# Performance work log

Hardware: AMD Instinct MI355X
Metric: run time of the kernel (lower is better)

The kernel has to match this reference:

```python
import jax, jax.numpy as jnp
import numpy as np

N = 512       # building thermal nodes (state dim)
M = 9         # inputs: [Tout(t), Q_1..Q_8]
T = 20000     # RK4 grid points
DT = 30.0     # seconds per step (as in docstring example)
N_DATA = 2000 # outside-temperature breakpoints for interp


def setup_inputs() -> dict:
    key = jax.random.key(0)
    kA, kB, kQ, kT, kiv = jax.random.split(key, 5)
    # Stable continuous-time system: spectral radius ~5e-3 -> |lambda*dt| ~ 0.2
    A = (jax.random.normal(kA, (N, N), jnp.float32) * 1e-4
         - 5e-3 * jnp.eye(N, dtype=jnp.float32))
    B = jax.random.normal(kB, (N, M), jnp.float32) * 1e-3
    Q = jax.random.uniform(kQ, (M - 1,), jnp.float32) * 100.0  # heat gains
    t_eval = jnp.arange(T, dtype=jnp.float32) * DT
    # interp1d replacement: sorted breakpoints + diurnal temperature signal
    Tout_t = jnp.linspace(0.0, T * DT, N_DATA).astype(jnp.float32)
    Tout_v = (15.0 + 10.0 * jnp.sin(2.0 * jnp.pi * Tout_t / 86400.0)
              + jax.random.normal(kT, (N_DATA,), jnp.float32))
    iv = 20.0 + jax.random.normal(kiv, (N,), jnp.float32)
    return {"A": A, "B": B, "Q": Q, "Tout_t": Tout_t, "Tout_v": Tout_v,
            "iv": iv, "t_eval": t_eval}


def reference(A, B, Q, Tout_t, Tout_v, iv, t_eval):
    """RK4 (torchdiffeq 3/8-rule fixed-grid) integration of dx/dt = A@x + B@u(t)."""

    def f(t, x):
        Tout = jnp.interp(t, Tout_t, Tout_v)          # on-device interp1d
        u = jnp.concatenate([Tout[None], Q])          # [M]
        return A @ x + B @ u                          # [N]

    def step(x, td):
        t, dt = td
        k1 = f(t, x)
        k2 = f(t + dt / 3.0, x + dt * k1 / 3.0)
        k3 = f(t + dt * 2.0 / 3.0, x + dt * (k2 - k1 / 3.0))
        k4 = f(t + dt, x + dt * (k1 - k2 + k3))
        x_new = x + dt * (k1 + 3.0 * (k2 + k3) + k4) / 8.0
        return x_new, x_new

    ts = t_eval[:-1]
    dts = jnp.diff(t_eval)
    _, xs = jax.lax.scan(step, iv, (ts, dts))         # [T-1, N]
    return jnp.concatenate([iv[None, :], xs], axis=0)  # [T, N]
```

## Files before the change

kernel.cpp:

```cpp
#include <hip/hip_runtime.h>

#define TT    20000
#define CCH   2500
#define RROWS 2501
#define NDATA 2000
#define MSZ   262144

typedef unsigned short u16;
typedef unsigned int   u32;
using f32x4 = __attribute__((ext_vector_type(4))) float;
using s16x8 = __attribute__((ext_vector_type(8))) short;

static constexpr size_t OFF_HT  = 0;
static constexpr size_t OFF_H2T = (size_t)MSZ;
static constexpr size_t OFF_MP  = 2*(size_t)MSZ;
static constexpr size_t OFF_SQ  = 10*(size_t)MSZ;
static constexpr size_t OFF_VEC = 12*(size_t)MSZ;
static constexpr size_t OFF_FJ  = OFF_VEC + 4096;
static constexpr size_t OFF_AL  = OFF_FJ + 163840;
static constexpr size_t OFF_SA  = OFF_AL + 102400;
static constexpr size_t OFF_SB  = OFF_SA + (size_t)RROWS*512;

__device__ __forceinline__ u16 f2bf(float f) {
    u32 u = __float_as_uint(f);
    u += 0x7fff + ((u >> 16) & 1);
    return (u16)(u >> 16);
}

#define MICRO_FMA(a, b) do { \
  acc0.x += (a).x*(b).x; acc0.y += (a).x*(b).y; acc0.z += (a).x*(b).z; acc0.w += (a).x*(b).w; \
  acc1.x += (a).y*(b).x; acc1.y += (a).y*(b).y; acc1.z += (a).y*(b).z; acc1.w += (a).y*(b).w; \
  acc2.x += (a).z*(b).x; acc2.y += (a).z*(b).y; acc2.z += (a).z*(b).z; acc2.w += (a).z*(b).w; \
  acc3.x += (a).w*(b).x; acc3.y += (a).w*(b).y; acc3.z += (a).w*(b).z; acc3.w += (a).w*(b).w; \
} while (0)

#define DECL_GEMM_VARS() \
    int t = threadIdx.x; \
    int tx = t & 15, ty = t >> 4; \
    int ar = t & 63, ak4 = (t >> 6) * 4; \
    int bk = t >> 4, bc4 = (t & 15) * 4; \
    float4 acc0 = {0,0,0,0}, acc1 = {0,0,0,0}, acc2 = {0,0,0,0}, acc3 = {0,0,0,0}; \
    (void)tx; (void)ty; (void)ar; (void)ak4; (void)bk; (void)bc4

#define GEMM_CORE_DB(LOADA, LOADB) \
    { float4 ra = LOADA(0); float4 rbv = LOADB(0); \
    As[0][ak4+0][ar]=ra.x; As[0][ak4+1][ar]=ra.y; As[0][ak4+2][ar]=ra.z; As[0][ak4+3][ar]=ra.w; \
    *(float4*)&Bs[0][bk][bc4] = rbv; \
    for (int kt = 1; kt <= 32; kt++) { \
        __syncthreads(); \
        const int cur = (kt - 1) & 1; \
        if (kt < 32) { ra = LOADA(kt); rbv = LOADB(kt); } \
        _Pragma("unroll") \
        for (int kk = 0; kk < 16; kk++) { \
            float4 a = *(const float4*)&As[cur][kk][ty*4]; \
            float4 b = *(const float4*)&Bs[cur][kk][tx*4]; \
            MICRO_FMA(a, b); \
        } \
        if (kt < 32) { const int nb = kt & 1; \
            As[nb][ak4+0][ar]=ra.x; As[nb][ak4+1][ar]=ra.y; As[nb][ak4+2][ar]=ra.z; As[nb][ak4+3][ar]=ra.w; \
            *(float4*)&Bs[nb][bk][bc4] = rbv; } \
    } }

__device__ __forceinline__ void pow_tile(const float* __restrict__ Ap,
                                         const float* __restrict__ Bp,
                                         float* __restrict__ Zp, int idx) {
    __shared__ float As[2][16][68], Bs[2][16][68];
    DECL_GEMM_VARS();
    int rb = (idx >> 3) * 64, cb = (idx & 7) * 64;
#define LA(kt) (*(const float4*)&Ap[(size_t)(rb+ar)*512 + (kt)*16 + ak4])
#define LB(kt) (*(const float4*)&Bp[(size_t)((kt)*16+bk)*512 + cb + bc4])
    GEMM_CORE_DB(LA, LB)
#undef LA
#undef LB
    size_t zb = (size_t)(rb + ty*4)*512 + cb + tx*4;
    *(float4*)&Zp[zb]        = acc0;
    *(float4*)&Zp[zb + 512]  = acc1;
    *(float4*)&Zp[zb + 1024] = acc2;
    *(float4*)&Zp[zb + 1536] = acc3;
}

__device__ __forceinline__ void matvecT128(const float* __restrict__ MT,
                                           const float* __restrict__ x,
                                           float* __restrict__ y, int rb,
                                           const float* __restrict__ gc,
                                           const float* __restrict__ gu1,
                                           const float* __restrict__ gu2) {
    __shared__ float xs[512];
    __shared__ float red2[2][128];
    int t = threadIdx.x;
    xs[t] = x[t]; xs[t + 256] = x[t + 256];
    __syncthreads();
    int rl = t & 127, h = t >> 7;
    size_t col = (size_t)rb + rl;
    float acc = 0.f;
    int k0 = h << 8;
    #pragma unroll 4
    for (int k = k0; k < k0 + 256; k++) acc += MT[(size_t)k*512 + col] * xs[k];
    red2[h][rl] = acc;
    __syncthreads();
    if (t < 128) {
        float s = red2[0][t] + red2[1][t];
        int r = rb + t;
        if (gc) y[r] = 30.f * (gc[r] + 0.5f*gu1[r] + (1.f/6.f)*gu2[r] + (1.f/24.f)*s);
        else    y[r] = s;
    }
}

__device__ __forceinline__ float interp1(float tt, const float* __restrict__ xp,
                                         const float* __restrict__ fp) {
    if (tt <= xp[0]) return fp[0];
    if (tt >= xp[NDATA-1]) return fp[NDATA-1];
    int lo = 0, hi = NDATA - 1;
    while (hi - lo > 1) { int mid = (lo + hi) >> 1; if (xp[mid] <= tt) lo = mid; else hi = mid; }
    float x0 = xp[lo], x1 = xp[lo+1];
    return fp[lo] + (fp[lo+1] - fp[lo]) * (tt - x0) / (x1 - x0);
}

__global__ __launch_bounds__(256) void k_setup(const float* __restrict__ A,
        const float* __restrict__ B, const float* __restrict__ Q,
        const float* __restrict__ te, const float* __restrict__ Tt,
        const float* __restrict__ Tv, const float* __restrict__ iv,
        float* __restrict__ HT, float* __restrict__ vec, float* __restrict__ AL,
        float* __restrict__ out, float* __restrict__ SA) {
    int bx = blockIdx.x, t = threadIdx.x;
    if (bx < 256) {
        __shared__ float Ts[32][33];
        int tr = bx >> 4, tc = bx & 15;
        int rl = t >> 3, cl4 = (t & 7) * 4;
        float4 a = *(const float4*)&A[(size_t)(tr*32 + rl)*512 + tc*32 + cl4];
        Ts[rl][cl4+0] = 30.f*a.x; Ts[rl][cl4+1] = 30.f*a.y;
        Ts[rl][cl4+2] = 30.f*a.z; Ts[rl][cl4+3] = 30.f*a.w;
        __syncthreads();
        float4 o;
        o.x = Ts[cl4+0][rl]; o.y = Ts[cl4+1][rl]; o.z = Ts[cl4+2][rl]; o.w = Ts[cl4+3][rl];
        *(float4*)&HT[(size_t)(tc*32 + rl)*512 + tr*32 + cl4] = o;
    } else if (bx == 256) {
        for (int i = t; i < 512; i += 256) {
            float v = B[i*9];
            float c = 0.f;
            #pragma unroll
            for (int j = 0; j < 8; j++) c += B[i*9 + 1 + j] * Q[j];
            vec[i] = v;
            vec[2560 + i] = c;
        }
    } else if (bx == 257) {
        for (int i = t; i < 512; i += 256) { out[i] = iv[i]; SA[i] = iv[i]; }
    } else {
        int n = (bx - 258) * 256 + t;
        if (n >= TT) return;
        float* a = AL + (size_t)n * 5;
        if (n == TT - 1) { a[0]=a[1]=a[2]=a[3]=a[4]=0.f; return; }
        float tt = te[n];
        float T1 = interp1(tt, Tt, Tv);
        float T2 = interp1(tt + 10.f, Tt, Tv);
        float T3 = interp1(tt + 20.f, Tt, Tv);
        float T4 = interp1(tt + 30.f, Tt, Tv);
        a[0] = 3.75f * (T1 + 3.f*T2 + 3.f*T3 + T4);
        a[1] = 3.75f * (T1 + 2.f*T2 + T3);
        a[2] = 3.75f * (T1*(1.f/3.f) + T2);
        a[3] = 1.25f * T1;
        a[4] = 1.f;
    }
}

__global__ __launch_bounds__(256) void k_h2kv(const float* __restrict__ HT,
                                              float* __restrict__ H2T,
                                              float* __restrict__ vec) {
    int bx = blockIdx.x;
    if (bx < 64) { pow_tile(HT, HT, H2T, bx); return; }
    int sub = bx - 64, which = sub >> 2, rb = (sub & 3) * 128;
    if (which == 0) matvecT128(HT, vec,        vec + 512,  rb, 0, 0, 0);
    else            matvecT128(HT, vec + 2560, vec + 3072, rb, 0, 0, 0);
}

__global__ __launch_bounds__(256) void k_m1kv(const float* __restrict__ HT,
                                              const float* __restrict__ H2T,
                                              float* __restrict__ M1T,
                                              float* __restrict__ vec) {
    int bx = blockIdx.x;
    if (bx < 64) {
        __shared__ float As[2][16][68], Bs[2][16][68];
        DECL_GEMM_VARS();
        int rb = (bx >> 3) * 64, cb = (bx & 7) * 64;
#define LA(kt) ({ size_t off = (size_t)(rb+ar)*512 + (kt)*16 + ak4; \
        float4 h  = *(const float4*)&HT[off]; \
        float4 h2 = *(const float4*)&H2T[off]; \
        float4 r_; \
        r_.x = h.x*(1.f/6.f) + h2.x*(1.f/24.f); r_.y = h.y*(1.f/6.f) + h2.y*(1.f/24.f); \
        r_.z = h.z*(1.f/6.f) + h2.z*(1.f/24.f); r_.w = h.w*(1.f/6.f) + h2.w*(1.f/24.f); \
        int dd = (rb+ar) - ((kt)*16 + ak4); \
        if (dd >= 0 && dd < 4) (&r_.x)[dd] += 0.5f; \
        r_; })
#define LB(kt) (*(const float4*)&H2T[(size_t)((kt)*16+bk)*512 + cb + bc4])
        GEMM_CORE_DB(LA, LB)
#undef LA
#undef LB
        int col = cb + tx*4;
        #pragma unroll
        for (int i = 0; i < 4; i++) {
            int r = rb + ty*4 + i;
            float4 h = *(const float4*)&HT[(size_t)r*512 + col];
            float4* ac = (i==0) ? &acc0 : (i==1) ? &acc1 : (i==2) ? &acc2 : &acc3;
            ac->x += h.x + (r == col+0 ? 1.f : 0.f);
            ac->y += h.y + (r == col+1 ? 1.f : 0.f);
            ac->z += h.z + (r == col+2 ? 1.f : 0.f);
            ac->w += h.w + (r == col+3 ? 1.f : 0.f);
            *(float4*)&M1T[(size_t)r*512 + col] = *ac;
        }
        return;
    }
    int sub = bx - 64, which = sub >> 2, rb = (sub & 3) * 128;
    if (which == 0) matvecT128(HT, vec + 512,  vec + 1024, rb, 0, 0, 0);
    else            matvecT128(HT, vec + 3072, vec + 3584, rb, 0, 0, 0);
}

__global__ __launch_bounds__(256) void k_m2kv(const float* __restrict__ M1T,
                                              float* __restrict__ M2T,
                                              const float* __restrict__ HT,
                                              float* __restrict__ vec) {
    int bx = blockIdx.x;
    if (bx < 64) { pow_tile(M1T, M1T, M2T, bx); return; }
    int sub = bx - 64, which = sub >> 2, rb = (sub & 3) * 128;
    if (which == 0) matvecT128(HT, vec + 1024, vec + 1536, rb, 0, 0, 0);
    else matvecT128(HT, vec + 3584, vec + 2048, rb,
                    vec + 2560, vec + 3072, vec + 3584);
}

__global__ __launch_bounds__(256) void k_pow(const float* __restrict__ A,
                                             const float* __restrict__ B0,
                                             float* __restrict__ Z0) {
    int sel = blockIdx.x >> 6;
    pow_tile(A, B0 + (size_t)sel*MSZ, Z0 + (size_t)sel*MSZ, blockIdx.x & 63);
}

__global__ __launch_bounds__(256) void k_wgen_sq(const float* __restrict__ vec,
                                                 const float* __restrict__ MP,
                                                 float* __restrict__ FJ,
                                                 const float* __restrict__ P,
                                                 float* __restrict__ Pout) {
    int bx = blockIdx.x;
    if (bx >= 64) { pow_tile(P, P, Pout, bx - 64); return; }
    int d = bx >> 3, cb = (bx & 7) * 64;
    int t = threadIdx.x;
    if (d == 0) {
        for (int idx = t; idx < 320; idx += 256) {
            int r = idx >> 6, c = idx & 63;
            float s = vec[(size_t)r*512 + cb + c];
            #pragma unroll
            for (int i = 0; i < 8; i++)
                FJ[((size_t)i*40 + i*5 + r)*512 + cb + c] = s;
        }
        for (int j = 0; j < 7; j++)
            for (int i = j + 1; i < 8; i++)
                for (int idx = t; idx < 320; idx += 256) {
                    int r = idx >> 6, c = idx & 63;
                    FJ[((size_t)j*40 + i*5 + r)*512 + cb + c] = 0.f;
                }
        return;
    }
    __shared__ float Ws[5][512];
    __shared__ float red4[4][5][64];
    const float* Mj = MP + (size_t)(d - 1)*MSZ;
    for (int e = t; e < 2560; e += 256) Ws[e >> 9][e & 511] = vec[e];
    __syncthreads();
    int col = t & 63, kq = t >> 6, k0 = kq * 128;
    float acc[5] = {0.f, 0.f, 0.f, 0.f, 0.f};
    #pragma unroll 4
    for (int k = k0; k < k0 + 128; k++) {
        float m = Mj[(size_t)k*512 + cb + col];
        acc[0] += Ws[0][k]*m; acc[1] += Ws[1][k]*m; acc[2] += Ws[2][k]*m;
        acc[3] += Ws[3][k]*m; acc[4] += Ws[4][k]*m;
    }
    #pragma unroll
    for (int r = 0; r < 5; r++) red4[kq][r][col] = acc[r];
    __syncthreads();
    for (int idx = t; idx < 320; idx += 256) {
        int r = idx >> 6, c = idx & 63;
        float s = red4[0][r][c] + red4[1][r][c] + red4[2][r][c] + red4[3][r][c];
        for (int i = 0; i + d < 8; i++)
            FJ[((size_t)(i + d)*40 + i*5 + r)*512 + cb + c] = s;
    }
}

__global__ __launch_bounds__(256) void k_e40_sq(const float* __restrict__ AL,
                                                const float* __restrict__ FJ,
                                                float* __restrict__ SA1,
                                                const float* __restrict__ P,
                                                float* __restrict__ Pout) {
    int bx = blockIdx.x;
    if (bx >= 320) { pow_tile(P, P, Pout, bx - 320); return; }
    const float* GT = FJ + (size_t)7*40*512;
    int kb = (bx >> 3) * 64, cb = (bx & 7) * 64;
    __shared__ float Ah[64][41], Bsv[40][68];
    int t = threadIdx.x;
    int tx = t & 15, ty = t >> 4;
    #pragma unroll
    for (int m = 0; m < 10; m++) {
        int e = t + 256*m;
        int row = e / 40, q = e - 40*row;
        float v = 0.f;
        if (kb + row < CCH) v = AL[(size_t)(kb + row)*40 + q];
        Ah[row][q] = v;
        int fq = e >> 6, fc = e & 63;
        Bsv[fq][fc] = GT[(size_t)fq*512 + cb + fc];
    }
    __syncthreads();
    float4 acc0 = {0,0,0,0}, acc1 = {0,0,0,0}, acc2 = {0,0,0,0}, acc3 = {0,0,0,0};
    #pragma unroll 8
    for (int q = 0; q < 40; q++) {
        float4 b = *(const float4*)&Bsv[q][tx*4];
        float a0 = Ah[ty*4+0][q], a1 = Ah[ty*4+1][q];
        float a2 = Ah[ty*4+2][q], a3 = Ah[ty*4+3][q];
        acc0.x += a0*b.x; acc0.y += a0*b.y; acc0.z += a0*b.z; acc0.w += a0*b.w;
        acc1.x += a1*b.x; acc1.y += a1*b.y; acc1.z += a1*b.z; acc1.w += a1*b.w;
        acc2.x += a2*b.x; acc2.y += a2*b.y; acc2.z += a2*b.z; acc2.w += a2*b.w;
        acc3.x += a3*b.x; acc3.y += a3*b.y; acc3.z += a3*b.z; acc3.w += a3*b.w;
    }
    int col = cb + tx*4;
    #pragma unroll
    for (int i = 0; i < 4; i++) {
        int k = kb + ty*4 + i;
        if (k < CCH) {
            float4 a = (i==0) ? acc0 : (i==1) ? acc1 : (i==2) ? acc2 : acc3;
            *(float4*)&SA1[(size_t)k*512 + col] = a;
        }
    }
}

__global__ __launch_bounds__(256) void k_scan_sq(const float* __restrict__ Ain,
                                                 float* __restrict__ Aout,
                                                 const float* __restrict__ QT, int shift,
                                                 const float* __restrict__ P,
                                                 float* __restrict__ Pout) {
    int bx = blockIdx.x;
    if (bx >= 320) { pow_tile(P, P, Pout, bx - 320); return; }
    __shared__ float As[2][16][68], Bs[2][16][68];
    DECL_GEMM_VARS();
    int kb = (bx >> 3) * 64, cb = (bx & 7) * 64;
    int xr = kb + ar - shift;
    bool aval = (xr >= 0) && (kb + ar < RROWS);
#define LA(kt) ({ float4 z = {0,0,0,0}; \
        if (aval) z = *(const float4*)&Ain[(size_t)xr*512 + (kt)*16 + ak4]; z; })
#define LB(kt) (*(const float4*)&QT[(size_t)((kt)*16+bk)*512 + cb + bc4])
    GEMM_CORE_DB(LA, LB)
#undef LA
#undef LB
    int col = cb + tx*4;
    #pragma unroll
    for (int i = 0; i < 4; i++) {
        int krow = kb + ty*4 + i;
        if (krow < RROWS) {
            float4 own = *(const float4*)&Ain[(size_t)krow*512 + col];
            float4 a = (i==0) ? acc0 : (i==1) ? acc1 : (i==2) ? acc2 : acc3;
            float4 res = {own.x + a.x, own.y + a.y, own.z + a.z, own.w + a.w};
            *(float4*)&Aout[(size_t)krow*512 + col] = res;
        }
    }
}

__global__ __launch_bounds__(256) void k_mprep(const float* __restrict__ MPin,
                                               u16* __restrict__ Mbf,
                                               const float* __restrict__ FJ,
                                               float* __restrict__ FJT) {
    int bx = blockIdx.x;
    int t = threadIdx.x;
    if (bx >= 512) {
        int bx2 = bx - 512;
        int j = bx2 >> 1, half = bx2 & 1;
        int col = half*256 + t;
        const float* Fb = FJ + (size_t)j*40*512 + col;
        float* Ft = FJT + (size_t)j*512*40 + (size_t)col*40;
        #pragma unroll 8
        for (int q = 0; q < 40; q++) Ft[q] = Fb[(size_t)q*512];
        return;
    }
    int j = bx >> 6, tile = bx & 63;
    int kb = (tile >> 3) * 64, cb = (tile & 7) * 64;
    const float* MT = MPin + (size_t)j * MSZ;
    __shared__ float Ts[64][65];
    int lr = t >> 4, lc = (t & 15) * 4;
    #pragma unroll
    for (int p = 0; p < 4; p++) {
        float4 v = *(const float4*)&MT[(size_t)(kb + p*16 + lr)*512 + cb + lc];
        Ts[p*16+lr][lc+0] = v.x; Ts[p*16+lr][lc+1] = v.y;
        Ts[p*16+lr][lc+2] = v.z; Ts[p*16+lr][lc+3] = v.w;
    }
    __syncthreads();
    int r = t >> 2, c16 = (t & 3) * 16;
    u32 pk[8];
    #pragma unroll
    for (int i = 0; i < 8; i++) {
        u32 a = f2bf(Ts[c16 + 2*i][r]);
        u32 b = f2bf(Ts[c16 + 2*i + 1][r]);
        pk[i] = a | (b << 16);
    }
    u16* dst = Mbf + (size_t)j*MSZ + (size_t)(cb + r)*512 + kb + c16;
    *(uint4*)dst       = make_uint4(pk[0], pk[1], pk[2], pk[3]);
    *(uint4*)(dst + 8) = make_uint4(pk[4], pk[5], pk[6], pk[7]);
}

__global__ __launch_bounds__(256, 2) void k_final(const float* __restrict__ SS,
                                               const u16* __restrict__ Mbf,
                                               const float* __restrict__ AL,
                                               const float* __restrict__ FJT,
                                               float* __restrict__ out) {
    __shared__ u16 Bsu[512*36];
    __shared__ u16 Asu[32*36];
    __shared__ float Ah[32][40];
    int t = threadIdx.x;
    int lane = t & 63, w = t >> 6;
    int lo16 = lane & 15, hi = lane >> 4;
    int j = blockIdx.x;
    int kb = blockIdx.y * 32;

    int b_r  = t >> 2;
    int b_k8 = (t & 3) * 8;
    int a_r  = t >> 3;
    int a_c4 = (t & 7) * 4;
    const u16* Bb = Mbf + (size_t)j*MSZ;
    const float* Ab = SS + (size_t)(kb + a_r)*512 + a_c4;
    const bool aval = (kb + a_r) < CCH;

    f32x4 acc[2][8];
    #pragma unroll
    for (int m = 0; m < 2; m++)
        #pragma unroll
        for (int n = 0; n < 8; n++) acc[m][n] = 0.f;

    uint4 pb[8]; float4 pa;
#define PREFETCH(kt) do { \
    _Pragma("unroll") \
    for (int p = 0; p < 8; p++) \
        pb[p] = *(const uint4*)&Bb[(size_t)(p*64 + b_r)*512 + (kt)*32 + b_k8]; \
    const float4 z4_ = {0.f,0.f,0.f,0.f}; \
    pa = aval ? *(const float4*)&Ab[(kt)*32] : z4_; \
} while (0)
#define STORE_LDS() do { \
    _Pragma("unroll") \
    for (int p = 0; p < 8; p++) \
        *(uint4*)&Bsu[(p*64 + b_r)*36 + b_k8] = pb[p]; \
    uint2 pk_; \
    pk_.x = (u32)f2bf(pa.x) | ((u32)f2bf(pa.y) << 16); \
    pk_.y = (u32)f2bf(pa.z) | ((u32)f2bf(pa.w) << 16); \
    *(uint2*)&Asu[a_r*36 + a_c4] = pk_; \
} while (0)

    PREFETCH(0);
    for (int kt = 0; kt < 16; kt++) {
        __syncthreads();
        STORE_LDS();
        __syncthreads();
        if (kt < 15) PREFETCH(kt + 1);
        __builtin_amdgcn_sched_barrier(0);
        s16x8 fa0 = *(const s16x8*)&Asu[(lo16)*36 + hi*8];
        s16x8 fa1 = *(const s16x8*)&Asu[(16 + lo16)*36 + hi*8];
        #pragma unroll
        for (int n = 0; n < 8; n++) {
            s16x8 fb = *(const s16x8*)&Bsu[((size_t)(w*128 + n*16 + lo16))*36 + hi*8];
            acc[0][n] = __builtin_amdgcn_mfma_f32_16x16x32_bf16(fa0, fb, acc[0][n], 0, 0, 0);
            acc[1][n] = __builtin_amdgcn_mfma_f32_16x16x32_bf16(fa1, fb, acc[1][n], 0, 0, 0);
        }
    }
#undef PREFETCH
#undef STORE_LDS

    __syncthreads();
    for (int i = t; i < 1280; i += 256) {
        int row = i / 40, q = i - row*40;
        float v = 0.f;
        if (kb + row < CCH) v = AL[(size_t)(kb + row)*40 + q];
        (&Ah[0][0])[i] = v;
    }
    __syncthreads();
    const float* Ft = FJT + (size_t)j*512*40;
    int colb = w*128 + lo16;
    #pragma unroll 2
    for (int q4 = 0; q4 < 10; q4++) {
        float4 fv[8];
        #pragma unroll
        for (int n = 0; n < 8; n++)
            fv[n] = *(const float4*)&Ft[(size_t)(colb + n*16)*40 + q4*4];
        #pragma unroll
        for (int m = 0; m < 2; m++) {
            #pragma unroll
            for (int r = 0; r < 4; r++) {
                float4 av = *(const float4*)&Ah[m*16 + hi*4 + r][q4*4];
                #pragma unroll
                for (int n = 0; n < 8; n++)
                    acc[m][n][r] += av.x*fv[n].x + av.y*fv[n].y + av.z*fv[n].z + av.w*fv[n].w;
            }
        }
    }
    #pragma unroll
    for (int m = 0; m < 2; m++) {
        #pragma unroll
        for (int r = 0; r < 4; r++) {
            int k = kb + m*16 + hi*4 + r;
            int n_out = 8*k + j + 1;
            if (k < CCH && n_out < TT) {
                size_t ro = (size_t)n_out*512 + w*128 + lo16;
                #pragma unroll
                for (int n = 0; n < 8; n++)
                    out[ro + n*16] = acc[m][n][r];
            }
        }
    }
}

extern "C" void kernel_launch(void* const* d_in, const int* in_sizes, int n_in,
                              void* d_out, int out_size, void* d_ws, size_t ws_size,
                              hipStream_t stream) {
    const float* A  = (const float*)d_in[0];
    const float* B  = (const float*)d_in[1];
    const float* Q  = (const float*)d_in[2];
    const float* Tt = (const float*)d_in[3];
    const float* Tv = (const float*)d_in[4];
    const float* iv = (const float*)d_in[5];
    const float* te = (const float*)d_in[6];
    float* out = (float*)d_out;
    float* w = (float*)d_ws;

    float* HT  = w + OFF_HT;
    float* H2T = w + OFF_H2T;
    float* MP  = w + OFF_MP;
    float* SQ  = w + OFF_SQ;
    float* vec = w + OFF_VEC;
    float* FJ  = w + OFF_FJ;
    float* AL  = w + OFF_AL;
    float* SA  = w + OFF_SA;
    float* SB  = w + OFF_SB;

    float* M16 = H2T;
    float* M32 = HT;
    float* M64 = SQ;
    float* M8  = MP + 7*(size_t)MSZ;
    u16*   Mbf = (u16*)SB;
    float* FJT = SB + 4*(size_t)MSZ;

    k_setup<<<337, 256, 0, stream>>>(A, B, Q, te, Tt, Tv, iv, HT, vec, AL, out, SA);
    k_h2kv<<<72, 256, 0, stream>>>(HT, H2T, vec);
    k_m1kv<<<72, 256, 0, stream>>>(HT, H2T, MP, vec);
    k_m2kv<<<72, 256, 0, stream>>>(MP, MP + MSZ, HT, vec);
    k_pow<<<128, 256, 0, stream>>>(MP + MSZ, MP, MP + 2*(size_t)MSZ);
    k_pow<<<256, 256, 0, stream>>>(MP + 3*(size_t)MSZ, MP, MP + 4*(size_t)MSZ);
    k_wgen_sq<<<128, 256, 0, stream>>>(vec, MP, FJ, M8, M16);
    k_e40_sq<<<384, 256, 0, stream>>>(AL, FJ, SA + 512, M16, M32);
    k_scan_sq<<<384, 256, 0, stream>>>(SA, SB, M8,  1, M32, M64);
    k_scan_sq<<<320, 256, 0, stream>>>(SB, SA, M16, 2, nullptr, nullptr);
    k_scan_sq<<<320, 256, 0, stream>>>(SA, SB, M32, 4, nullptr, nullptr);
    k_scan_sq<<<320, 256, 0, stream>>>(SB, SA, M64, 8, nullptr, nullptr);
    k_mprep<<<528, 256, 0, stream>>>(MP, Mbf, FJ, FJT);
    k_final<<<dim3(8, 79), 256, 0, stream>>>(SA, Mbf, AL, FJT, out);
}
```

Before: 537.0 us.

## Fold forcing-term correction into bf16 MFMA GEMM with pre-tiled operands

The fp32 FMA epilogue that added AL·FJ in k_final is replaced by extending the K dimension from 16 to 18 tiles, so AL and FJ are converted to bf16 and handled by the same MFMA loop. A new k_mprepA kernel pre-converts the state rows and AL into a kt-major bf16 tiled layout, and B is repacked per k-tile, making prefetch loads contiguous and removing per-iteration conversion. Output is staged through LDS so the stores write full rows as float4. This adds an extra launch and lowers the correction term's precision to bf16, and occupancy is raised to 3 blocks per CU.

```diff
diff --git a/kernel.cpp b/kernel.cpp
--- a/kernel.cpp
+++ b/kernel.cpp
@@ -20,6 +20,8 @@
 static constexpr size_t OFF_AL  = OFF_FJ + 163840;
 static constexpr size_t OFF_SA  = OFF_AL + 102400;
 static constexpr size_t OFF_SB  = OFF_SA + (size_t)RROWS*512;
+
+#define KTN 18
 
 __device__ __forceinline__ u16 f2bf(float f) {
     u32 u = __float_as_uint(f);
@@ -358,20 +360,35 @@
     }
 }
 
-__global__ __launch_bounds__(256) void k_mprep(const float* __restrict__ MPin,
-                                               u16* __restrict__ Mbf,
-                                               const float* __restrict__ FJ,
-                                               float* __restrict__ FJT) {
+__global__ __launch_bounds__(256) void k_mprepB(const float* __restrict__ MPin,
+                                                u16* __restrict__ Mbf2,
+                                                const float* __restrict__ FJ) {
     int bx = blockIdx.x;
     int t = threadIdx.x;
     if (bx >= 512) {
         int bx2 = bx - 512;
         int j = bx2 >> 1, half = bx2 & 1;
         int col = half*256 + t;
-        const float* Fb = FJ + (size_t)j*40*512 + col;
-        float* Ft = FJT + (size_t)j*512*40 + (size_t)col*40;
+        u16 arr[64];
         #pragma unroll 8
-        for (int q = 0; q < 40; q++) Ft[q] = Fb[(size_t)q*512];
+        for (int q = 0; q < 64; q++) {
+            float v = (q < 40) ? FJ[((size_t)j*40 + q)*512 + col] : 0.f;
+            arr[q] = f2bf(v);
+        }
+        #pragma unroll
+        for (int qh = 0; qh < 2; qh++) {
+            u16* d = Mbf2 + ((size_t)(j*KTN + 16 + qh)*512 + col)*32;
+            #pragma unroll
+            for (int i = 0; i < 4; i++) {
+                int b0 = qh*32 + i*8;
+                uint4 P;
+                P.x = (u32)arr[b0+0] | ((u32)arr[b0+1] << 16);
+                P.y = (u32)arr[b0+2] | ((u32)arr[b0+3] << 16);
+                P.z = (u32)arr[b0+4] | ((u32)arr[b0+5] << 16);
+                P.w = (u32)arr[b0+6] | ((u32)arr[b0+7] << 16);
+                *(uint4*)(d + i*8) = P;
+            }
+        }
         return;
     }
     int j = bx >> 6, tile = bx & 63;
@@ -394,63 +411,92 @@
         u32 b = f2bf(Ts[c16 + 2*i + 1][r]);
         pk[i] = a | (b << 16);
     }
-    u16* dst = Mbf + (size_t)j*MSZ + (size_t)(cb + r)*512 + kb + c16;
+    int ktg = (kb + c16) >> 5;
+    u16* dst = Mbf2 + ((size_t)(j*KTN + ktg)*512 + cb + r)*32 + (c16 & 16);
     *(uint4*)dst       = make_uint4(pk[0], pk[1], pk[2], pk[3]);
     *(uint4*)(dst + 8) = make_uint4(pk[4], pk[5], pk[6], pk[7]);
 }
 
-__global__ __launch_bounds__(256, 2) void k_final(const float* __restrict__ SS,
-                                               const u16* __restrict__ Mbf,
-                                               const float* __restrict__ AL,
-                                               const float* __restrict__ FJT,
+__global__ __launch_bounds__(256) void k_mprepA(const float* __restrict__ SS,
+                                                const float* __restrict__ AL,
+                                                u16* __restrict__ A2) {
+    int g = blockIdx.x * 256 + threadIdx.x;
+    if (g >= 2528 * KTN * 2) return;
+    int half = g & 1;
+    int rk = g >> 1;
+    int k = rk % 2528;
+    int kt = rk / 2528;
+    u16 o[16];
+    if (kt < 16) {
+        if (k < CCH) {
+            const float* src = SS + (size_t)k*512 + kt*32 + half*16;
+            #pragma unroll
+            for (int i = 0; i < 16; i++) o[i] = f2bf(src[i]);
+        } else {
+            #pragma unroll
+            for (int i = 0; i < 16; i++) o[i] = 0;
+        }
+    } else {
+        int q0 = (kt - 16)*32 + half*16;
+        #pragma unroll
+        for (int i = 0; i < 16; i++) {
+            int q = q0 + i;
+            float v = (k < CCH && q < 40) ? AL[(size_t)k*40 + q] : 0.f;
+            o[i] = f2bf(v);
+        }
+    }
+    u16* d = A2 + ((size_t)kt*2528 + k)*32 + half*16;
+    uint4 P0, P1;
+    P0.x = (u32)o[0]  | ((u32)o[1]  << 16); P0.y = (u32)o[2]  | ((u32)o[3]  << 16);
+    P0.z = (u32)o[4]  | ((u32)o[5]  << 16); P0.w = (u32)o[6]  | ((u32)o[7]  << 16);
+    P1.x = (u32)o[8]  | ((u32)o[9]  << 16); P1.y = (u32)o[10] | ((u32)o[11] << 16);
+    P1.z = (u32)o[12] | ((u32)o[13] << 16); P1.w = (u32)o[14] | ((u32)o[15] << 16);
+    *(uint4*)d       = P0;
+    *(uint4*)(d + 8) = P1;
+}
+
+__global__ __launch_bounds__(256, 3) void k_final(const u16* __restrict__ A2,
+                                               const u16* __restrict__ Mbf2,
                                                float* __restrict__ out) {
-    __shared__ u16 Bsu[512*36];
-    __shared__ u16 Asu[32*36];
-    __shared__ float Ah[32][40];
+    __shared__ char smem[39168];
+    u16* Bsu = (u16*)smem;
+    u16* Asu = (u16*)(smem + 36864);
     int t = threadIdx.x;
     int lane = t & 63, w = t >> 6;
     int lo16 = lane & 15, hi = lane >> 4;
     int j = blockIdx.x;
     int kb = blockIdx.y * 32;
 
-    int b_r  = t >> 2;
-    int b_k8 = (t & 3) * 8;
-    int a_r  = t >> 3;
-    int a_c4 = (t & 7) * 4;
-    const u16* Bb = Mbf + (size_t)j*MSZ;
-    const float* Ab = SS + (size_t)(kb + a_r)*512 + a_c4;
-    const bool aval = (kb + a_r) < CCH;
-
     f32x4 acc[2][8];
     #pragma unroll
     for (int m = 0; m < 2; m++)
         #pragma unroll
         for (int n = 0; n < 8; n++) acc[m][n] = 0.f;
 
-    uint4 pb[8]; float4 pa;
+    const u16* Bj = Mbf2 + (size_t)j*KTN*16384;
+    const u16* Ab = A2 + (size_t)kb*32;
+
+    uint4 pb[8]; uint4 pa;
 #define PREFETCH(kt) do { \
+    const u16* Bs_ = Bj + (size_t)(kt)*16384; \
     _Pragma("unroll") \
     for (int p = 0; p < 8; p++) \
-        pb[p] = *(const uint4*)&Bb[(size_t)(p*64 + b_r)*512 + (kt)*32 + b_k8]; \
-    const float4 z4_ = {0.f,0.f,0.f,0.f}; \
-    pa = aval ? *(const float4*)&Ab[(kt)*32] : z4_; \
+        pb[p] = *(const uint4*)&Bs_[(w*8 + p)*512 + lane*8]; \
+    if (t < 128) pa = *(const uint4*)&Ab[(size_t)(kt)*2528*32 + t*8]; \
 } while (0)
 #define STORE_LDS() do { \
     _Pragma("unroll") \
     for (int p = 0; p < 8; p++) \
-        *(uint4*)&Bsu[(p*64 + b_r)*36 + b_k8] = pb[p]; \
-    uint2 pk_; \
-    pk_.x = (u32)f2bf(pa.x) | ((u32)f2bf(pa.y) << 16); \
-    pk_.y = (u32)f2bf(pa.z) | ((u32)f2bf(pa.w) << 16); \
-    *(uint2*)&Asu[a_r*36 + a_c4] = pk_; \
+        *(uint4*)&Bsu[((w*8 + p)*16 + (lane>>2))*36 + (lane&3)*8] = pb[p]; \
+    if (t < 128) *(uint4*)&Asu[(t>>2)*36 + (t&3)*8] = pa; \
 } while (0)
 
     PREFETCH(0);
-    for (int kt = 0; kt < 16; kt++) {
+    for (int kt = 0; kt < KTN; kt++) {
         __syncthreads();
         STORE_LDS();
         __syncthreads();
-        if (kt < 15) PREFETCH(kt + 1);
+        if (kt < KTN-1) PREFETCH(kt + 1);
         __builtin_amdgcn_sched_barrier(0);
         s16x8 fa0 = *(const s16x8*)&Asu[(lo16)*36 + hi*8];
         s16x8 fa1 = *(const s16x8*)&Asu[(16 + lo16)*36 + hi*8];
@@ -464,45 +510,27 @@
 #undef PREFETCH
 #undef STORE_LDS
 
-    __syncthreads();
-    for (int i = t; i < 1280; i += 256) {
-        int row = i / 40, q = i - row*40;
-        float v = 0.f;
-        if (kb + row < CCH) v = AL[(size_t)(kb + row)*40 + q];
-        (&Ah[0][0])[i] = v;
-    }
-    __syncthreads();
-    const float* Ft = FJT + (size_t)j*512*40;
-    int colb = w*128 + lo16;
-    #pragma unroll 2
-    for (int q4 = 0; q4 < 10; q4++) {
-        float4 fv[8];
-        #pragma unroll
-        for (int n = 0; n < 8; n++)
-            fv[n] = *(const float4*)&Ft[(size_t)(colb + n*16)*40 + q4*4];
-        #pragma unroll
-        for (int m = 0; m < 2; m++) {
+    float* ldsT = (float*)smem;
+    #pragma unroll
+    for (int m = 0; m < 2; m++) {
+        __syncthreads();
+        #pragma unroll
+        for (int r = 0; r < 4; r++) {
+            int rl = hi*4 + r;
             #pragma unroll
-            for (int r = 0; r < 4; r++) {
-                float4 av = *(const float4*)&Ah[m*16 + hi*4 + r][q4*4];
-                #pragma unroll
-                for (int n = 0; n < 8; n++)
-                    acc[m][n][r] += av.x*fv[n].x + av.y*fv[n].y + av.z*fv[n].z + av.w*fv[n].w;
-            }
-        }
-    }
-    #pragma unroll
-    for (int m = 0; m < 2; m++) {
-        #pragma unroll
-        for (int r = 0; r < 4; r++) {
-            int k = kb + m*16 + hi*4 + r;
+            for (int n = 0; n < 8; n++)
+                ldsT[rl*516 + w*128 + n*16 + lo16] = acc[m][n][r];
+        }
+        __syncthreads();
+        #pragma unroll
+        for (int p = 0; p < 8; p++) {
+            int idx = t + p*256;
+            int row = idx >> 7, c4 = idx & 127;
+            int k = kb + m*16 + row;
             int n_out = 8*k + j + 1;
-            if (k < CCH && n_out < TT) {
-                size_t ro = (size_t)n_out*512 + w*128 + lo16;
-                #pragma unroll
-                for (int n = 0; n < 8; n++)
-                    out[ro + n*16] = acc[m][n][r];
-            }
+            if (k < CCH && n_out < TT)
+                *(float4*)&out[(size_t)n_out*512 + c4*4] =
+                    *(const float4*)&ldsT[row*516 + c4*4];
         }
     }
 }
@@ -534,8 +562,8 @@
     float* M32 = HT;
     float* M64 = SQ;
     float* M8  = MP + 7*(size_t)MSZ;
-    u16*   Mbf = (u16*)SB;
-    float* FJT = SB + 4*(size_t)MSZ;
+    u16*   Mbf2 = (u16*)SB;
+    u16*   A2   = (u16*)w;
 
     k_setup<<<337, 256, 0, stream>>>(A, B, Q, te, Tt, Tv, iv, HT, vec, AL, out, SA);
     k_h2kv<<<72, 256, 0, stream>>>(HT, H2T, vec);
@@ -549,6 +577,7 @@
     k_scan_sq<<<320, 256, 0, stream>>>(SB, SA, M16, 2, nullptr, nullptr);
     k_scan_sq<<<320, 256, 0, stream>>>(SA, SB, M32, 4, nullptr, nullptr);
     k_scan_sq<<<320, 256, 0, stream>>>(SB, SA, M64, 8, nullptr, nullptr);
-    k_mprep<<<528, 256, 0, stream>>>(MP, Mbf, FJ, FJT);
-    k_final<<<dim3(8, 79), 256, 0, stream>>>(SA, Mbf, AL, FJT, out);
-}
+    k_mprepB<<<528, 256, 0, stream>>>(MP, Mbf2, FJ);
+    k_mprepA<<<356, 256, 0, stream>>>(SA, AL, A2);
+    k_final<<<dim3(8, 79), 256, 0, stream>>>(A2, Mbf2, out);
+}
```

Result: slower. 570.4 us (+6.2%).
